# Kernel optimization log

Hardware: AMD Instinct MI355X
Metric: run time of the kernel (lower is better)

Reference implementation:

```python
import jax, jax.numpy as jnp
import numpy as np

B, V, G, D = 16, 16384, 20000, 64


def setup_inputs() -> dict:
    key = jax.random.key(0)
    k1, k2 = jax.random.split(key)
    variant_embeddings = jax.random.normal(k1, (B, V, D), dtype=jnp.float32)
    gene_ids = jax.random.randint(k2, (B, V), 0, G, dtype=jnp.int64)
    mask = jnp.ones((B, V), dtype=bool)
    return {
        "variant_embeddings": variant_embeddings,
        "gene_ids": gene_ids,
        "mask": mask,
        "num_genes": G,
    }


def reference(variant_embeddings, gene_ids, mask, num_genes):
    # Aggregation = 'max'. Genes with no valid variants -> zero embedding.
    b, v, d = variant_embeddings.shape
    # Flatten (batch, variant) and build per-(batch,gene) segment ids.
    seg = (jnp.arange(b, dtype=gene_ids.dtype)[:, None] * num_genes + gene_ids).reshape(-1)
    m = mask.reshape(-1)
    # Route padded variants to a dummy trailing segment so they never contribute.
    dummy = b * num_genes
    seg = jnp.where(m, seg, dummy)
    x = variant_embeddings.reshape(b * v, d)  # mask-zeroing is a no-op for selected (valid) rows under max
    num_segments = b * num_genes + 1
    mx = jax.ops.segment_max(x, seg, num_segments=num_segments)[: b * num_genes]  # [b*G, d]
    counts = jax.ops.segment_sum(m.astype(x.dtype), seg, num_segments=num_segments)[: b * num_genes]  # [b*G]
    out = jnp.where(counts[:, None] > 0, mx, jnp.zeros((), dtype=x.dtype))
    return out.reshape(b, num_genes, d)
```

## Files before the change

### kernel.cpp

```cpp
#include <hip/hip_runtime.h>

constexpr int B = 16;
constexpr int V = 16384;
constexpr int G = 20000;
constexpr int D = 64;
constexpr int NCELLS = B * G;
constexpr int NROWS  = B * V;
constexpr int OVF_MAX = 16384;
constexpr long long OUT_N = (long long)NCELLS * D;

constexpr int OVF_HDR   = NCELLS;
constexpr int OVF_LIST  = NCELLS + 1;
constexpr int LISTS_OFF = NCELLS + 1 + 2 * OVF_MAX;

__global__ void ga_zero(unsigned int* __restrict__ ws, int n) {
  int stride = gridDim.x * blockDim.x;
  for (int i = blockIdx.x * blockDim.x + threadIdx.x; i < n; i += stride)
    ws[i] = 0u;
}

__global__ void ga_build(const int* __restrict__ gene_ids,
                         const int* __restrict__ mask,
                         unsigned int* __restrict__ ws, int cap) {
  int r = blockIdx.x * blockDim.x + threadIdx.x;
  if (r >= NROWS) return;
  if (!mask[r]) return;
  int b = r >> 14;
  int cell = b * G + gene_ids[r];
  unsigned int pos = atomicAdd(&ws[cell], 1u);
  if (pos < (unsigned int)cap) {
    ws[LISTS_OFF + (size_t)cell * cap + pos] = (unsigned int)r;
  } else {
    unsigned int o = atomicAdd(&ws[OVF_HDR], 1u);
    if (o < (unsigned int)OVF_MAX) {
      ws[OVF_LIST + 2 * o + 0] = (unsigned int)cell;
      ws[OVF_LIST + 2 * o + 1] = (unsigned int)r;
    }
  }
}

__global__ void ga_gather(const float4* __restrict__ emb4,
                          const unsigned int* __restrict__ ws,
                          float4* __restrict__ out4, int cap) {
  int t = blockIdx.x * blockDim.x + threadIdx.x;
  int cell = t >> 4;
  int sub  = t & 15;
  if (cell >= NCELLS) return;
  unsigned int c = ws[cell];
  int n = (int)(c < (unsigned int)cap ? c : (unsigned int)cap);
  const unsigned int* lp = ws + LISTS_OFF + (size_t)cell * cap;
  float ninf = -__builtin_inff();
  float4 acc = make_float4(ninf, ninf, ninf, ninf);
  for (int k = 0; k < n; ++k) {
    unsigned int row = lp[k];
    float4 v = emb4[(size_t)row * 16 + sub];
    acc.x = fmaxf(acc.x, v.x);
    acc.y = fmaxf(acc.y, v.y);
    acc.z = fmaxf(acc.z, v.z);
    acc.w = fmaxf(acc.w, v.w);
  }
  if (c == 0u) acc = make_float4(0.f, 0.f, 0.f, 0.f);
  out4[(size_t)cell * 16 + sub] = acc;
}

__device__ __forceinline__ void atomic_max_float(float* addr, float val) {
  unsigned int* ua = (unsigned int*)addr;
  unsigned int old = *ua;
  while (__uint_as_float(old) < val) {
    unsigned int assumed = old;
    old = atomicCAS(ua, assumed, __float_as_uint(val));
    if (old == assumed) break;
  }
}

__global__ void ga_ovf(const float4* __restrict__ emb4,
                       const unsigned int* __restrict__ ws,
                       float* __restrict__ out) {
  unsigned int nov = ws[OVF_HDR];
  if (nov > (unsigned int)OVF_MAX) nov = OVF_MAX;
  int total = (int)nov * 16;
  int stride = gridDim.x * blockDim.x;
  for (int u = blockIdx.x * blockDim.x + threadIdx.x; u < total; u += stride) {
    int e = u >> 4, sub = u & 15;
    unsigned int cell = ws[OVF_LIST + 2 * e + 0];
    unsigned int row  = ws[OVF_LIST + 2 * e + 1];
    float4 v = emb4[(size_t)row * 16 + sub];
    float* o = out + (size_t)cell * 64 + sub * 4;
    atomic_max_float(o + 0, v.x);
    atomic_max_float(o + 1, v.y);
    atomic_max_float(o + 2, v.z);
    atomic_max_float(o + 3, v.w);
  }
}

__device__ __forceinline__ unsigned int enc_f32(float f) {
  unsigned int u = __float_as_uint(f);
  return (u & 0x80000000u) ? ~u : (u | 0x80000000u);
}
__device__ __forceinline__ float dec_f32(unsigned int e) {
  unsigned int u = (e & 0x80000000u) ? (e ^ 0x80000000u) : ~e;
  return __uint_as_float(u);
}

__global__ void ga_init(uint4* __restrict__ out4, int n4) {
  int stride = gridDim.x * blockDim.x;
  for (int i = blockIdx.x * blockDim.x + threadIdx.x; i < n4; i += stride)
    out4[i] = make_uint4(0u, 0u, 0u, 0u);
}

__global__ void ga_scatter(const float4* __restrict__ emb4,
                           const int* __restrict__ gene_ids,
                           const int* __restrict__ mask,
                           unsigned int* __restrict__ out) {
  int tid = blockIdx.x * blockDim.x + threadIdx.x;
  int v  = tid >> 4;
  int dq = tid & 15;
  if (!mask[v]) return;
  int g = gene_ids[v];
  int b = v >> 14;
  float4 e = emb4[tid];
  int base = (b * G + g) * D + (dq << 2);
  atomicMax(out + base + 0, enc_f32(e.x));
  atomicMax(out + base + 1, enc_f32(e.y));
  atomicMax(out + base + 2, enc_f32(e.z));
  atomicMax(out + base + 3, enc_f32(e.w));
}

__global__ void ga_finalize(uint4* __restrict__ io4, int n4) {
  int stride = gridDim.x * blockDim.x;
  for (int i = blockIdx.x * blockDim.x + threadIdx.x; i < n4; i += stride) {
    uint4 e = io4[i];
    float4 f;
    f.x = e.x ? dec_f32(e.x) : 0.0f;
    f.y = e.y ? dec_f32(e.y) : 0.0f;
    f.z = e.z ? dec_f32(e.z) : 0.0f;
    f.w = e.w ? dec_f32(e.w) : 0.0f;
    *reinterpret_cast<float4*>(io4 + i) = f;
  }
}

extern "C" void kernel_launch(void* const* d_in, const int* in_sizes, int n_in,
                              void* d_out, int out_size, void* d_ws, size_t ws_size,
                              hipStream_t stream) {
  const float4* emb4     = (const float4*)d_in[0];
  const int*    gene_ids = (const int*)d_in[1];
  const int*    mask     = (const int*)d_in[2];

  long long ws_u32 = (long long)(ws_size / 4);
  long long avail  = ws_u32 - (long long)LISTS_OFF;
  int cap = (int)(avail > 0 ? avail / NCELLS : 0);
  if (cap > 16) cap = 16;

  if (cap >= 6) {
    unsigned int* ws = (unsigned int*)d_ws;
    ga_zero<<<512, 256, 0, stream>>>(ws, NCELLS + 1);
    ga_build<<<NROWS / 256, 256, 0, stream>>>(gene_ids, mask, ws, cap);
    ga_gather<<<(int)(OUT_N / 4 / 256), 256, 0, stream>>>(
        emb4, ws, (float4*)d_out, cap);
    ga_ovf<<<64, 256, 0, stream>>>(emb4, ws, (float*)d_out);
  } else {
    unsigned int* out_u = (unsigned int*)d_out;
    const int n4 = (int)(OUT_N / 4);
    ga_init<<<2048, 256, 0, stream>>>((uint4*)d_out, n4);
    ga_scatter<<<(NROWS * 16) / 256, 256, 0, stream>>>(emb4, gene_ids, mask, out_u);
    ga_finalize<<<2048, 256, 0, stream>>>((uint4*)d_out, n4);
  }
}
```

Measured before the change: 53.86 us.

## Inline first three rows per cell in a 16-byte header with spill lists

Each cell now gets a 16-byte header holding its count and the first three row indices, so the gather kernel reads one uint4 per cell instead of a count plus a separate list. Longer lists spill to a secondary area. Each gather thread also handles four cells, loading all four headers up front to raise memory-level parallelism, and empty cells skip the -inf setup. The header area is four times larger to zero, and the ws size condition for taking this path changes.

Measured after the change: 49.64 us. 7.8% less time.

```diff
diff --git a/kernel.cpp b/kernel.cpp
--- a/kernel.cpp
+++ b/kernel.cpp
@@ -9,27 +9,30 @@
 constexpr int OVF_MAX = 16384;
 constexpr long long OUT_N = (long long)NCELLS * D;
 
-constexpr int OVF_HDR   = NCELLS;
-constexpr int OVF_LIST  = NCELLS + 1;
-constexpr int LISTS_OFF = NCELLS + 1 + 2 * OVF_MAX;
+constexpr int HDR_WORDS = 4 * NCELLS;
+constexpr int OVF_HDR   = HDR_WORDS;
+constexpr int OVF_LIST  = HDR_WORDS + 1;
+constexpr int SPILL_OFF = HDR_WORDS + 1 + 2 * OVF_MAX;
 
-__global__ void ga_zero(unsigned int* __restrict__ ws, int n) {
+__global__ void ga_zero(uint4* __restrict__ ws4, unsigned int* __restrict__ ws) {
   int stride = gridDim.x * blockDim.x;
-  for (int i = blockIdx.x * blockDim.x + threadIdx.x; i < n; i += stride)
-    ws[i] = 0u;
+  for (int i = blockIdx.x * blockDim.x + threadIdx.x; i < HDR_WORDS / 4; i += stride)
+    ws4[i] = make_uint4(0u, 0u, 0u, 0u);
+  if (blockIdx.x == 0 && threadIdx.x == 0) ws[OVF_HDR] = 0u;
 }
 
 __global__ void ga_build(const int* __restrict__ gene_ids,
                          const int* __restrict__ mask,
-                         unsigned int* __restrict__ ws, int cap) {
+                         unsigned int* __restrict__ ws, int scap) {
   int r = blockIdx.x * blockDim.x + threadIdx.x;
   if (r >= NROWS) return;
   if (!mask[r]) return;
-  int b = r >> 14;
-  int cell = b * G + gene_ids[r];
-  unsigned int pos = atomicAdd(&ws[cell], 1u);
-  if (pos < (unsigned int)cap) {
-    ws[LISTS_OFF + (size_t)cell * cap + pos] = (unsigned int)r;
+  int cell = (r >> 14) * G + gene_ids[r];
+  unsigned int pos = atomicAdd(&ws[cell * 4], 1u);
+  if (pos < 3u) {
+    ws[cell * 4 + 1 + pos] = (unsigned int)r;
+  } else if (pos < 3u + (unsigned int)scap) {
+    ws[SPILL_OFF + (size_t)cell * scap + (pos - 3u)] = (unsigned int)r;
   } else {
     unsigned int o = atomicAdd(&ws[OVF_HDR], 1u);
     if (o < (unsigned int)OVF_MAX) {
@@ -39,28 +42,48 @@
   }
 }
 
+__device__ __forceinline__ void fmax4(float4& a, float4 v) {
+  a.x = fmaxf(a.x, v.x);
+  a.y = fmaxf(a.y, v.y);
+  a.z = fmaxf(a.z, v.z);
+  a.w = fmaxf(a.w, v.w);
+}
+
+constexpr int CPT = 4;
 __global__ void ga_gather(const float4* __restrict__ emb4,
-                          const unsigned int* __restrict__ ws,
-                          float4* __restrict__ out4, int cap) {
+                          const uint4* __restrict__ hdr,
+                          const unsigned int* __restrict__ spill,
+                          float4* __restrict__ out4, int scap) {
+  const int N = NCELLS * 16 / CPT;
   int t = blockIdx.x * blockDim.x + threadIdx.x;
-  int cell = t >> 4;
-  int sub  = t & 15;
-  if (cell >= NCELLS) return;
-  unsigned int c = ws[cell];
-  int n = (int)(c < (unsigned int)cap ? c : (unsigned int)cap);
-  const unsigned int* lp = ws + LISTS_OFF + (size_t)cell * cap;
-  float ninf = -__builtin_inff();
-  float4 acc = make_float4(ninf, ninf, ninf, ninf);
-  for (int k = 0; k < n; ++k) {
-    unsigned int row = lp[k];
-    float4 v = emb4[(size_t)row * 16 + sub];
-    acc.x = fmaxf(acc.x, v.x);
-    acc.y = fmaxf(acc.y, v.y);
-    acc.z = fmaxf(acc.z, v.z);
-    acc.w = fmaxf(acc.w, v.w);
+  if (t >= N) return;
+  uint4 h[CPT];
+  int cell0 = t >> 4;
+  int sub   = t & 15;
+#pragma unroll
+  for (int k = 0; k < CPT; ++k)
+    h[k] = hdr[cell0 + k * (NCELLS / CPT)];
+#pragma unroll
+  for (int k = 0; k < CPT; ++k) {
+    int cell = cell0 + k * (NCELLS / CPT);
+    unsigned int c = h[k].x;
+    float4 acc = make_float4(0.f, 0.f, 0.f, 0.f);
+    if (c != 0u) {
+      float ninf = -__builtin_inff();
+      acc = make_float4(ninf, ninf, ninf, ninf);
+      float4 v0 = emb4[(size_t)h[k].y * 16 + sub];
+      fmax4(acc, v0);
+      if (c >= 2u) fmax4(acc, emb4[(size_t)h[k].z * 16 + sub]);
+      if (c >= 3u) fmax4(acc, emb4[(size_t)h[k].w * 16 + sub]);
+      if (c > 3u) {
+        int n1 = (int)c - 3; if (n1 > scap) n1 = scap;
+        const unsigned int* sp = spill + (size_t)cell * scap;
+        for (int j = 0; j < n1; ++j)
+          fmax4(acc, emb4[(size_t)sp[j] * 16 + sub]);
+      }
+    }
+    out4[(size_t)cell * 16 + sub] = acc;
   }
-  if (c == 0u) acc = make_float4(0.f, 0.f, 0.f, 0.f);
-  out4[(size_t)cell * 16 + sub] = acc;
 }
 
 __device__ __forceinline__ void atomic_max_float(float* addr, float val) {
@@ -147,16 +170,17 @@
   const int*    mask     = (const int*)d_in[2];
 
   long long ws_u32 = (long long)(ws_size / 4);
-  long long avail  = ws_u32 - (long long)LISTS_OFF;
-  int cap = (int)(avail > 0 ? avail / NCELLS : 0);
-  if (cap > 16) cap = 16;
+  long long avail  = ws_u32 - (long long)SPILL_OFF;
+  int scap = (int)(avail > 0 ? avail / NCELLS : -1);
+  if (scap > 13) scap = 13;
 
-  if (cap >= 6) {
+  if (scap >= 0) {
     unsigned int* ws = (unsigned int*)d_ws;
-    ga_zero<<<512, 256, 0, stream>>>(ws, NCELLS + 1);
-    ga_build<<<NROWS / 256, 256, 0, stream>>>(gene_ids, mask, ws, cap);
-    ga_gather<<<(int)(OUT_N / 4 / 256), 256, 0, stream>>>(
-        emb4, ws, (float4*)d_out, cap);
+    ga_zero<<<1024, 256, 0, stream>>>((uint4*)d_ws, ws);
+    ga_build<<<NROWS / 256, 256, 0, stream>>>(gene_ids, mask, ws, scap);
+    const int N = NCELLS * 16 / CPT;
+    ga_gather<<<N / 256, 256, 0, stream>>>(
+        emb4, (const uint4*)d_ws, ws + SPILL_OFF, (float4*)d_out, scap);
     ga_ovf<<<64, 256, 0, stream>>>(emb4, ws, (float*)d_out);
   } else {
     unsigned int* out_u = (unsigned int*)d_out;
```
